# Performance work log

Measured on AMD Instinct MI355X. Metric: run time of the kernel, lower is better.

## Reference

```python
import jax, jax.numpy as jnp
import numpy as np

HIDDEN = 1024
HEADS = 16
HEAD_DIM = HIDDEN // HEADS
SCALE = 1.0 / float(np.sqrt(HEAD_DIM))


def setup_inputs() -> dict:
    key = jax.random.key(0)
    k1, k2, k3, k4 = jax.random.split(key, 4)
    B, N, C = 4, 2048, HIDDEN
    x = jax.random.normal(k1, (B, N, C), dtype=jnp.float32)
    # nn.Linear(C, 3C, bias=False): y = x @ W_qkv where W_qkv is [C, 3C]
    w_qkv = jax.random.normal(k2, (C, 3 * C), dtype=jnp.float32) * (1.0 / np.sqrt(C))
    # nn.Linear(C, C) with bias
    w_out = jax.random.normal(k3, (C, C), dtype=jnp.float32) * (1.0 / np.sqrt(C))
    b_out = jax.random.normal(k4, (C,), dtype=jnp.float32) * 0.01
    return {"x": x, "w_qkv": w_qkv, "w_out": w_out, "b_out": b_out}


def reference(x, w_qkv, w_out, b_out):
    B, N, C = x.shape
    H, D = HEADS, HEAD_DIM
    qkv = jnp.einsum("bnc,cf->bnf", x, w_qkv)  # [B, N, 3C]
    qkv = qkv.reshape(B, N, 3, H, D).transpose(2, 0, 3, 1, 4)  # [3, B, H, N, D]
    q, k, v = qkv[0], qkv[1], qkv[2]
    attn = jnp.einsum("bhnd,bhmd->bhnm", q, k) * SCALE  # [B, H, N, N]
    attn = jax.nn.softmax(attn, axis=-1)
    # dropout is identity in eval mode
    out = jnp.einsum("bhnm,bhmd->bhnd", attn, v)  # [B, H, N, D]
    out = out.transpose(0, 2, 1, 3).reshape(B, N, C)
    return jnp.einsum("bnc,co->bno", out, w_out) + b_out
```

## Files before the change

kernel.cpp:

```cpp
#include <hip/hip_runtime.h>
#include <hip/hip_bf16.h>
#include <stdint.h>

#define SEQ   2048
#define NBH   64
#define DH    64
#define CH    1024
#define MTOT  8192
#define QSCALE 0.1803368801111204f

typedef __bf16 bf16_t;
typedef bf16_t bf16x8 __attribute__((ext_vector_type(8)));
typedef float  f32x4  __attribute__((ext_vector_type(4)));
typedef float  f32x16 __attribute__((ext_vector_type(16)));

__device__ __forceinline__ bf16_t to_bf16(float f) {
  uint32_t u = __builtin_bit_cast(uint32_t, f);
  uint16_t r = (uint16_t)((u + 0x7fffu + ((u >> 16) & 1u)) >> 16);
  return __builtin_bit_cast(bf16_t, r);
}

__device__ __forceinline__ void gload_lds16(const void* g, void* l) {
  __builtin_amdgcn_global_load_lds(
      (const __attribute__((address_space(1))) uint32_t*)g,
      (__attribute__((address_space(3))) uint32_t*)l, 16, 0, 0);
}

__device__ __forceinline__ f32x4 mfma_bf16(bf16x8 a, bf16x8 b, f32x4 c) {
  return __builtin_amdgcn_mfma_f32_16x16x32_bf16(a, b, c, 0, 0, 0);
}
__device__ __forceinline__ f32x16 mfma32_bf16(bf16x8 a, bf16x8 b, f32x16 c) {
  return __builtin_amdgcn_mfma_f32_32x32x16_bf16(a, b, c, 0, 0, 0);
}

__device__ __forceinline__ float exp2_fast(float x) {
#if __has_builtin(__builtin_amdgcn_exp2f)
  return __builtin_amdgcn_exp2f(x);
#else
  float r;
  asm("v_exp_f32 %0, %1\ns_nop 0" : "=v"(r) : "v"(x));
  return r;
#endif
}

__device__ __forceinline__ uint32_t cvt_pk_bf16(float lo, float hi) {
  uint32_t r;
  asm("v_cvt_pk_bf16_f32 %0, %1, %2" : "=v"(r) : "v"(lo), "v"(hi));
  return r;
}

__device__ __forceinline__ void permlane32_swap(uint32_t& a, uint32_t& b) {
  asm("s_nop 1\n\tv_permlane32_swap_b32 %0, %1\n\ts_nop 1" : "+v"(a), "+v"(b));
}

__global__ __launch_bounds__(256) void prep(
    const float* __restrict__ x, bf16_t* __restrict__ xb,
    const float* __restrict__ w_qkv, bf16_t* __restrict__ wqkvT,
    const float* __restrict__ w_out, bf16_t* __restrict__ woT) {
  __shared__ float t[64 * 65];
  const int tid = threadIdx.x;
  const int blk = blockIdx.x;
  if (blk < 2048) {
    int i = (blk * 256 + tid) * 4;
    const int stride = 2048 * 256 * 4;
    for (; i < MTOT * CH; i += stride) {
      const float4 f = *reinterpret_cast<const float4*>(x + i);
      bf16_t tmp[4] = {to_bf16(f.x), to_bf16(f.y), to_bf16(f.z), to_bf16(f.w)};
      *reinterpret_cast<uint2*>(xb + i) = *reinterpret_cast<uint2*>(tmp);
    }
    return;
  }
  const float* W; bf16_t* WT; int Nd, nx, bi;
  if (blk < 2048 + 768) { bi = blk - 2048; W = w_qkv; WT = wqkvT; Nd = 3 * CH; nx = 48; }
  else                  { bi = blk - 2816; W = w_out; WT = woT;   Nd = CH;     nx = 16; }
  const int n0 = (bi % nx) * 64, k0 = (bi / nx) * 64;
#pragma unroll
  for (int rr = 0; rr < 16; ++rr) {
    const int idx = rr * 256 + tid;
    const int r = idx >> 6, c = idx & 63;
    t[r * 65 + c] = W[(size_t)(k0 + r) * Nd + n0 + c];
  }
  __syncthreads();
#pragma unroll
  for (int rr = 0; rr < 16; ++rr) {
    const int idx = rr * 256 + tid;
    const int nr = idx >> 6, kc = idx & 63;
    WT[(size_t)(n0 + nr) * CH + k0 + kc] = to_bf16(t[kc * 65 + nr]);
  }
}


template <int EPI>
__global__ __launch_bounds__(256, 3) void gemm_bt(
    const bf16_t* __restrict__ A, const bf16_t* __restrict__ BT, int K, int nx,
    bf16_t* __restrict__ qb, bf16_t* __restrict__ kb, bf16_t* __restrict__ vb,
    const float* __restrict__ bias, float* __restrict__ out) {
  __shared__ __attribute__((aligned(16))) bf16_t lA[128 * 64];
  __shared__ __attribute__((aligned(16))) bf16_t lB[128 * 64];
  const int tid = threadIdx.x;
  const int lane = tid & 63;
  const int wv = tid >> 6;
  const int wm = wv >> 1, wn = wv & 1;

  const int nwg = gridDim.x;
  int bid = blockIdx.x;
  bid = (bid & 7) * (nwg >> 3) + (bid >> 3);
  const int m0 = (bid / nx) * 128, n0 = (bid % nx) * 128;

  const int l15 = lane & 15, l16 = lane >> 4;

  f32x4 acc[4][4] = {};

  const int srow = tid >> 3;
  const int sch = tid & 7;

  for (int kt = 0; kt < K; kt += 64) {
#pragma unroll
    for (int c = 0; c < 4; ++c) {
      const int row = c * 32 + srow;
      const int cs = sch ^ (row & 7);
      gload_lds16(A + (size_t)(m0 + row) * K + kt + cs * 8, &lA[c * 2048 + tid * 8]);
    }
#pragma unroll
    for (int c = 0; c < 4; ++c) {
      const int row = c * 32 + srow;
      const int cs = sch ^ (row & 7);
      gload_lds16(BT + (size_t)(n0 + row) * K + kt + cs * 8, &lB[c * 2048 + tid * 8]);
    }
    __syncthreads();
#pragma unroll
    for (int ks = 0; ks < 2; ++ks) {
      bf16x8 af[4], bfr[4];
#pragma unroll
      for (int i = 0; i < 4; ++i) {
        const int ar = wm * 64 + i * 16 + l15;
        const int cha = (ks * 4 + l16) ^ (ar & 7);
        af[i] = *reinterpret_cast<const bf16x8*>(&lA[ar * 64 + cha * 8]);
        const int br = wn * 64 + i * 16 + l15;
        const int chb = (ks * 4 + l16) ^ (br & 7);
        bfr[i] = *reinterpret_cast<const bf16x8*>(&lB[br * 64 + chb * 8]);
      }
#pragma unroll
      for (int i = 0; i < 4; ++i)
#pragma unroll
        for (int j = 0; j < 4; ++j)
          acc[i][j] = mfma_bf16(af[i], bfr[j], acc[i][j]);
    }
    __syncthreads();
  }

  if (EPI == 0) {
    const int f0 = n0 + wn * 64;
    const int three = f0 >> 10;
    if (three < 2) {
#pragma unroll
      for (int i = 0; i < 4; ++i) {
#pragma unroll
        for (int j = 0; j < 4; ++j) {
#pragma unroll
          for (int r = 0; r < 4; ++r) {
            const int m = m0 + wm * 64 + i * 16 + l16 * 4 + r;
            const int f = f0 + j * 16 + l15;
            const int h = (f >> 6) & 15, d = f & 63;
            const int bh = (m >> 11) * 16 + h;
            const int n = m & 2047;
            const float val = acc[i][j][r];
            if (three == 0)
              qb[((size_t)bh * SEQ + n) * DH + d] = to_bf16(val * QSCALE);
            else
              kb[((size_t)bh * SEQ + n) * DH + d] = to_bf16(val);
          }
        }
      }
    } else {
#pragma unroll
      for (int i = 0; i < 4; ++i) {
#pragma unroll
        for (int j = 0; j < 4; ++j) {
          const int m = m0 + wm * 64 + i * 16 + l16 * 4;
          const int f = f0 + j * 16 + l15;
          const int h = (f >> 6) & 15, d = f & 63;
          const int bh = (m >> 11) * 16 + h;
          const int n = m & 2047;
          const uint2 pk = make_uint2(cvt_pk_bf16(acc[i][j][0], acc[i][j][1]),
                                      cvt_pk_bf16(acc[i][j][2], acc[i][j][3]));
          *reinterpret_cast<uint2*>(&vb[((size_t)bh * DH + d) * SEQ + n]) = pk;
        }
      }
    }
  } else {
#pragma unroll
    for (int j = 0; j < 4; ++j) {
      const int cc = n0 + wn * 64 + j * 16 + l15;
      const float bb = bias[cc];
#pragma unroll
      for (int i = 0; i < 4; ++i) {
#pragma unroll
        for (int r = 0; r < 4; ++r) {
          const int m = m0 + wm * 64 + i * 16 + l16 * 4 + r;
          out[(size_t)m * CH + cc] = acc[i][j][r] + bb;
        }
      }
    }
  }
}

__global__ __launch_bounds__(256, 4) void attn_fwd(
    const bf16_t* __restrict__ Q, const bf16_t* __restrict__ K,
    const bf16_t* __restrict__ V, bf16_t* __restrict__ O) {
  __shared__ __attribute__((aligned(16))) bf16_t lK[2][64 * 64];
  __shared__ __attribute__((aligned(16))) bf16_t lV[2][64 * 64];
  const int tid = threadIdx.x;
  const int lane = tid & 63;
  const int wv = tid >> 6;
  const int l31 = lane & 31, hi = lane >> 5;

  const int lin = blockIdx.x;
  const int bh = (lin & 7) * 8 + ((lin >> 3) & 7);
  const int qb = lin >> 6;
  const int q0w = qb * 128 + wv * 32;

  const bf16_t* Qb = Q + (size_t)bh * SEQ * DH;
  const bf16_t* Kb = K + (size_t)bh * SEQ * DH;
  const bf16_t* Vb = V + (size_t)bh * DH * SEQ;

  bf16x8 qf[4];
#pragma unroll
  for (int ks = 0; ks < 4; ++ks)
    qf[ks] = *reinterpret_cast<const bf16x8*>(
        Qb + (size_t)(q0w + l31) * DH + ks * 16 + hi * 8);

  f32x16 o0 = {}, o1 = {};
  float rs0 = 0.f, rs1 = 0.f, rs2 = 0.f, rs3 = 0.f;

  const int srow = tid >> 3;
  const int sch = tid & 7;

  auto stage = [&](int buf, int kt0) {
#pragma unroll
    for (int c = 0; c < 2; ++c) {
      const int row = c * 32 + srow;
      const int cs = sch ^ (row & 7);
      gload_lds16(Kb + (size_t)(kt0 + row) * DH + cs * 8,
                  reinterpret_cast<char*>(&lK[buf][0]) + c * 4096 + tid * 16);
      gload_lds16(Vb + (size_t)row * SEQ + kt0 + cs * 8,
                  reinterpret_cast<char*>(&lV[buf][0]) + c * 4096 + tid * 16);
    }
  };

  stage(0, 0);
  __syncthreads();
  int cur = 0;

  for (int t = 0; t < SEQ / 64; ++t) {
    if (t + 1 < SEQ / 64) stage(cur ^ 1, (t + 1) * 64);

    f32x16 s0 = {}, s1 = {};
    __builtin_amdgcn_s_setprio(1);
#pragma unroll
    for (int ks = 0; ks < 4; ++ks) {
      {
        const int row = l31;
        const int ch = (ks * 2 + hi) ^ (row & 7);
        const bf16x8 kf = *reinterpret_cast<const bf16x8*>(
            reinterpret_cast<const char*>(&lK[cur][0]) + row * 128 + ch * 16);
        s0 = mfma32_bf16(kf, qf[ks], s0);
      }
      {
        const int row = 32 + l31;
        const int ch = (ks * 2 + hi) ^ (row & 7);
        const bf16x8 kf = *reinterpret_cast<const bf16x8*>(
            reinterpret_cast<const char*>(&lK[cur][0]) + row * 128 + ch * 16);
        s1 = mfma32_bf16(kf, qf[ks], s1);
      }
    }
    __builtin_amdgcn_s_setprio(0);

#pragma unroll
    for (int j = 0; j < 16; j += 4) {
      s0[j]     = exp2_fast(s0[j]);     rs0 += s0[j];
      s0[j + 1] = exp2_fast(s0[j + 1]); rs1 += s0[j + 1];
      s0[j + 2] = exp2_fast(s0[j + 2]); rs2 += s0[j + 2];
      s0[j + 3] = exp2_fast(s0[j + 3]); rs3 += s0[j + 3];
    }
#pragma unroll
    for (int j = 0; j < 16; j += 4) {
      s1[j]     = exp2_fast(s1[j]);     rs0 += s1[j];
      s1[j + 1] = exp2_fast(s1[j + 1]); rs1 += s1[j + 1];
      s1[j + 2] = exp2_fast(s1[j + 2]); rs2 += s1[j + 2];
      s1[j + 3] = exp2_fast(s1[j + 3]); rs3 += s1[j + 3];
    }

    bf16x8 pa[4];
    {
      uint32_t a0 = cvt_pk_bf16(s0[0], s0[1]),   b0 = cvt_pk_bf16(s0[4], s0[5]);
      uint32_t a1 = cvt_pk_bf16(s0[2], s0[3]),   b1 = cvt_pk_bf16(s0[6], s0[7]);
      uint32_t a2 = cvt_pk_bf16(s0[8], s0[9]),   b2 = cvt_pk_bf16(s0[12], s0[13]);
      uint32_t a3 = cvt_pk_bf16(s0[10], s0[11]), b3 = cvt_pk_bf16(s0[14], s0[15]);
      permlane32_swap(a0, b0);
      permlane32_swap(a1, b1);
      permlane32_swap(a2, b2);
      permlane32_swap(a3, b3);
      union { uint32_t u[4]; bf16x8 v; } ua, ub, uc, ud;
      ua.u[0] = a0; ua.u[1] = a1; ua.u[2] = b0; ua.u[3] = b1; pa[0] = ua.v;
      ub.u[0] = a2; ub.u[1] = a3; ub.u[2] = b2; ub.u[3] = b3; pa[1] = ub.v;
      uint32_t c0 = cvt_pk_bf16(s1[0], s1[1]),   d0 = cvt_pk_bf16(s1[4], s1[5]);
      uint32_t c1 = cvt_pk_bf16(s1[2], s1[3]),   d1 = cvt_pk_bf16(s1[6], s1[7]);
      uint32_t c2 = cvt_pk_bf16(s1[8], s1[9]),   d2 = cvt_pk_bf16(s1[12], s1[13]);
      uint32_t c3 = cvt_pk_bf16(s1[10], s1[11]), d3 = cvt_pk_bf16(s1[14], s1[15]);
      permlane32_swap(c0, d0);
      permlane32_swap(c1, d1);
      permlane32_swap(c2, d2);
      permlane32_swap(c3, d3);
      uc.u[0] = c0; uc.u[1] = c1; uc.u[2] = d0; uc.u[3] = d1; pa[2] = uc.v;
      ud.u[0] = c2; ud.u[1] = c3; ud.u[2] = d2; ud.u[3] = d3; pa[3] = ud.v;
    }

    __builtin_amdgcn_s_setprio(1);
#pragma unroll
    for (int tt = 0; tt < 4; ++tt) {
      {
        const int row = l31;
        const int ch = (tt * 2 + hi) ^ (row & 7);
        const bf16x8 vf = *reinterpret_cast<const bf16x8*>(
            reinterpret_cast<const char*>(&lV[cur][0]) + row * 128 + ch * 16);
        o0 = mfma32_bf16(pa[tt], vf, o0);
      }
      {
        const int row = 32 + l31;
        const int ch = (tt * 2 + hi) ^ (row & 7);
        const bf16x8 vf = *reinterpret_cast<const bf16x8*>(
            reinterpret_cast<const char*>(&lV[cur][0]) + row * 128 + ch * 16);
        o1 = mfma32_bf16(pa[tt], vf, o1);
      }
    }
    __builtin_amdgcn_s_setprio(0);

    __syncthreads();
    cur ^= 1;
  }

  const float rs = (rs0 + rs1) + (rs2 + rs3);
  uint32_t ra = __builtin_bit_cast(uint32_t, rs), rb2 = ra;
  permlane32_swap(ra, rb2);
  const float tot = __builtin_bit_cast(float, ra) + __builtin_bit_cast(float, rb2);
  const float rinv = 1.0f / tot;

  const int b = bh >> 4, h = bh & 15;
#pragma unroll
  for (int r = 0; r < 16; ++r) {
    const int qr = (r & 3) + 8 * (r >> 2) + 4 * hi;
    const float inv = __shfl(rinv, qr, 64);
    const size_t grow = (size_t)(b * SEQ + q0w + qr) * CH + h * DH;
    O[grow + l31]      = to_bf16(o0[r] * inv);
    O[grow + 32 + l31] = to_bf16(o1[r] * inv);
  }
}


extern "C" void kernel_launch(void* const* d_in, const int* in_sizes, int n_in,
                              void* d_out, int out_size, void* d_ws, size_t ws_size,
                              hipStream_t stream) {
  const float* x     = (const float*)d_in[0];
  const float* w_qkv = (const float*)d_in[1];
  const float* w_out = (const float*)d_in[2];
  const float* b_out = (const float*)d_in[3];
  float* out = (float*)d_out;

  char* ws = (char*)d_ws;
  bf16_t* xb    = (bf16_t*)(ws);
  bf16_t* wqkvT = (bf16_t*)(ws + 16777216);
  bf16_t* woT   = (bf16_t*)(ws + 23068672);
  bf16_t* Qb    = (bf16_t*)(ws + 25165824);
  bf16_t* Kb    = (bf16_t*)(ws + 41943040);
  bf16_t* Vb    = (bf16_t*)(ws + 58720256);
  bf16_t* Ab    = xb;

  prep<<<3072, 256, 0, stream>>>(x, xb, w_qkv, wqkvT, w_out, woT);

  gemm_bt<0><<<(3 * CH / 128) * (MTOT / 128), 256, 0, stream>>>(
      xb, wqkvT, CH, 3 * CH / 128, Qb, Kb, Vb, nullptr, nullptr);

  attn_fwd<<<1024, 256, 0, stream>>>(Qb, Kb, Vb, Ab);

  gemm_bt<1><<<(CH / 128) * (MTOT / 128), 256, 0, stream>>>(
      Ab, woT, CH, CH / 128, nullptr, nullptr, nullptr, b_out, out);
}
```

Before: 167.8 us.

## Double-buffer GEMM LDS loads with 256x128 tiles and 512-thread blocks

Restructures the bf16 GEMM kernel to use 256x128 output tiles computed by 8 waves, with two LDS buffers so the global-to-LDS loads for tile k+2 overlap the MFMA work on tile k. Raw s_waitcnt/s_barrier sequences and s_setprio replace __syncthreads to control the pipeline, and K is hardcoded to CH. The cost is 96KB of LDS and one block per CU, which lowers occupancy, and the grid shrinks (e.g. 256 blocks for the output projection), which may underfill the CUs.

After: 190.2 us. 13.4% more time.

```diff
diff --git a/kernel.cpp b/kernel.cpp
--- a/kernel.cpp
+++ b/kernel.cpp
@@ -89,77 +89,98 @@
   }
 }
 
-
 template <int EPI>
-__global__ __launch_bounds__(256, 3) void gemm_bt(
-    const bf16_t* __restrict__ A, const bf16_t* __restrict__ BT, int K, int nx,
+__global__ __launch_bounds__(512, 1) void gemm_bt(
+    const bf16_t* __restrict__ A, const bf16_t* __restrict__ BT, int nx,
     bf16_t* __restrict__ qb, bf16_t* __restrict__ kb, bf16_t* __restrict__ vb,
     const float* __restrict__ bias, float* __restrict__ out) {
-  __shared__ __attribute__((aligned(16))) bf16_t lA[128 * 64];
-  __shared__ __attribute__((aligned(16))) bf16_t lB[128 * 64];
+  __shared__ __attribute__((aligned(16))) bf16_t lA[2][256 * 64];
+  __shared__ __attribute__((aligned(16))) bf16_t lB[2][128 * 64];
   const int tid = threadIdx.x;
   const int lane = tid & 63;
   const int wv = tid >> 6;
-  const int wm = wv >> 1, wn = wv & 1;
+  const int wr = wv >> 2, wc = wv & 3;
+  const int l15 = lane & 15, l16 = lane >> 4;
 
   const int nwg = gridDim.x;
   int bid = blockIdx.x;
   bid = (bid & 7) * (nwg >> 3) + (bid >> 3);
-  const int m0 = (bid / nx) * 128, n0 = (bid % nx) * 128;
-
-  const int l15 = lane & 15, l16 = lane >> 4;
-
-  f32x4 acc[4][4] = {};
+  const int m0 = (bid / nx) * 256, n0 = (bid % nx) * 128;
+
+  f32x4 acc[8][2] = {};
 
   const int srow = tid >> 3;
   const int sch = tid & 7;
 
-  for (int kt = 0; kt < K; kt += 64) {
+  auto stage = [&](int buf, int kt) {
 #pragma unroll
     for (int c = 0; c < 4; ++c) {
-      const int row = c * 32 + srow;
+      const int row = c * 64 + srow;
       const int cs = sch ^ (row & 7);
-      gload_lds16(A + (size_t)(m0 + row) * K + kt + cs * 8, &lA[c * 2048 + tid * 8]);
-    }
-#pragma unroll
-    for (int c = 0; c < 4; ++c) {
-      const int row = c * 32 + srow;
+      gload_lds16(A + (size_t)(m0 + row) * CH + kt + cs * 8,
+                  reinterpret_cast<char*>(&lA[buf][0]) + c * 8192 + tid * 16);
+    }
+#pragma unroll
+    for (int c = 0; c < 2; ++c) {
+      const int row = c * 64 + srow;
       const int cs = sch ^ (row & 7);
-      gload_lds16(BT + (size_t)(n0 + row) * K + kt + cs * 8, &lB[c * 2048 + tid * 8]);
-    }
-    __syncthreads();
-#pragma unroll
-    for (int ks = 0; ks < 2; ++ks) {
-      bf16x8 af[4], bfr[4];
-#pragma unroll
-      for (int i = 0; i < 4; ++i) {
-        const int ar = wm * 64 + i * 16 + l15;
-        const int cha = (ks * 4 + l16) ^ (ar & 7);
-        af[i] = *reinterpret_cast<const bf16x8*>(&lA[ar * 64 + cha * 8]);
-        const int br = wn * 64 + i * 16 + l15;
-        const int chb = (ks * 4 + l16) ^ (br & 7);
-        bfr[i] = *reinterpret_cast<const bf16x8*>(&lB[br * 64 + chb * 8]);
-      }
-#pragma unroll
-      for (int i = 0; i < 4; ++i)
-#pragma unroll
-        for (int j = 0; j < 4; ++j)
-          acc[i][j] = mfma_bf16(af[i], bfr[j], acc[i][j]);
-    }
-    __syncthreads();
+      gload_lds16(BT + (size_t)(n0 + row) * CH + kt + cs * 8,
+                  reinterpret_cast<char*>(&lB[buf][0]) + c * 8192 + tid * 16);
+    }
+  };
+
+  stage(0, 0);
+  stage(1, 64);
+
+  for (int kt = 0; kt < 16; ++kt) {
+    if (kt < 15)
+      asm volatile("s_waitcnt vmcnt(6)\n\ts_barrier" ::: "memory");
+    else
+      asm volatile("s_waitcnt vmcnt(0)\n\ts_barrier" ::: "memory");
+    const char* lap = reinterpret_cast<const char*>(&lA[kt & 1][0]);
+    const char* lbp = reinterpret_cast<const char*>(&lB[kt & 1][0]);
+
+    __builtin_amdgcn_s_setprio(1);
+    bf16x8 bfr[2][2];
+#pragma unroll
+    for (int j = 0; j < 2; ++j) {
+      const int br = wc * 32 + j * 16 + l15;
+#pragma unroll
+      for (int ks = 0; ks < 2; ++ks) {
+        const int ch = (ks * 4 + l16) ^ (br & 7);
+        bfr[j][ks] = *reinterpret_cast<const bf16x8*>(lbp + br * 128 + ch * 16);
+      }
+    }
+#pragma unroll
+    for (int i = 0; i < 8; ++i) {
+      const int ar = wr * 128 + i * 16 + l15;
+      const int ch0 = l16 ^ (ar & 7);
+      const bf16x8 af0 = *reinterpret_cast<const bf16x8*>(lap + ar * 128 + ch0 * 16);
+      const int ch1 = (4 + l16) ^ (ar & 7);
+      const bf16x8 af1 = *reinterpret_cast<const bf16x8*>(lap + ar * 128 + ch1 * 16);
+#pragma unroll
+      for (int j = 0; j < 2; ++j) {
+        acc[i][j] = mfma_bf16(af0, bfr[j][0], acc[i][j]);
+        acc[i][j] = mfma_bf16(af1, bfr[j][1], acc[i][j]);
+      }
+    }
+    __builtin_amdgcn_s_setprio(0);
+
+    asm volatile("s_barrier" ::: "memory");
+    if (kt + 2 < 16) stage(kt & 1, (kt + 2) * 64);
   }
 
   if (EPI == 0) {
-    const int f0 = n0 + wn * 64;
-    const int three = f0 >> 10;
+    const int f0 = n0 + wc * 32;
+    const int three = n0 >> 10;
     if (three < 2) {
 #pragma unroll
-      for (int i = 0; i < 4; ++i) {
-#pragma unroll
-        for (int j = 0; j < 4; ++j) {
+      for (int i = 0; i < 8; ++i) {
+#pragma unroll
+        for (int j = 0; j < 2; ++j) {
 #pragma unroll
           for (int r = 0; r < 4; ++r) {
-            const int m = m0 + wm * 64 + i * 16 + l16 * 4 + r;
+            const int m = m0 + wr * 128 + i * 16 + l16 * 4 + r;
             const int f = f0 + j * 16 + l15;
             const int h = (f >> 6) & 15, d = f & 63;
             const int bh = (m >> 11) * 16 + h;
@@ -174,10 +195,10 @@
       }
     } else {
 #pragma unroll
-      for (int i = 0; i < 4; ++i) {
-#pragma unroll
-        for (int j = 0; j < 4; ++j) {
-          const int m = m0 + wm * 64 + i * 16 + l16 * 4;
+      for (int i = 0; i < 8; ++i) {
+#pragma unroll
+        for (int j = 0; j < 2; ++j) {
+          const int m = m0 + wr * 128 + i * 16 + l16 * 4;
           const int f = f0 + j * 16 + l15;
           const int h = (f >> 6) & 15, d = f & 63;
           const int bh = (m >> 11) * 16 + h;
@@ -190,14 +211,14 @@
     }
   } else {
 #pragma unroll
-    for (int j = 0; j < 4; ++j) {
-      const int cc = n0 + wn * 64 + j * 16 + l15;
+    for (int j = 0; j < 2; ++j) {
+      const int cc = n0 + wc * 32 + j * 16 + l15;
       const float bb = bias[cc];
 #pragma unroll
-      for (int i = 0; i < 4; ++i) {
+      for (int i = 0; i < 8; ++i) {
 #pragma unroll
         for (int r = 0; r < 4; ++r) {
-          const int m = m0 + wm * 64 + i * 16 + l16 * 4 + r;
+          const int m = m0 + wr * 128 + i * 16 + l16 * 4 + r;
           out[(size_t)m * CH + cc] = acc[i][j][r] + bb;
         }
       }
@@ -378,11 +399,11 @@
 
   prep<<<3072, 256, 0, stream>>>(x, xb, w_qkv, wqkvT, w_out, woT);
 
-  gemm_bt<0><<<(3 * CH / 128) * (MTOT / 128), 256, 0, stream>>>(
-      xb, wqkvT, CH, 3 * CH / 128, Qb, Kb, Vb, nullptr, nullptr);
+  gemm_bt<0><<<(MTOT / 256) * (3 * CH / 128), 512, 0, stream>>>(
+      xb, wqkvT, 3 * CH / 128, Qb, Kb, Vb, nullptr, nullptr);
 
   attn_fwd<<<1024, 256, 0, stream>>>(Qb, Kb, Vb, Ab);
 
-  gemm_bt<1><<<(CH / 128) * (MTOT / 128), 256, 0, stream>>>(
-      Ab, woT, CH, CH / 128, nullptr, nullptr, nullptr, b_out, out);
-}
+  gemm_bt<1><<<(MTOT / 256) * (CH / 128), 512, 0, stream>>>(
+      Ab, woT, CH / 128, nullptr, nullptr, nullptr, b_out, out);
+}
```
